# Performance work log

Hardware: AMD Instinct MI355X
Metric: run time of the kernel (lower is better)

The kernel has to match this reference:

```python
import jax, jax.numpy as jnp
import numpy as np

B, D, H, L = 2, 1024, 16, 4
BLK = 16                 # block_size == max_text_tokens
MT, MF = 16, 2032        # max_text_tokens, max_font_tokens
S = MT + MF              # 2048
NB = S // BLK            # 128 blocks
V = 490                  # font_vocab_size
HD = D // H              # 64
WIN = 30                 # 3*max_glyph_tokens/block_size = 3*160/16
NGLOB, NRAND = 1, 2      # BigBird global / random blocks
SOS = 0.42


def _make_layout():
    # Deterministic BigBird block layout per head: [H, NB, NB] bool
    rng = np.random.default_rng(0)
    layout = np.zeros((H, NB, NB), dtype=bool)
    layout[:, :NGLOB, :] = True          # global rows
    layout[:, :, :NGLOB] = True          # global cols
    for i in range(NB):                  # sliding window
        layout[:, i, max(0, i - WIN // 2):min(NB, i + WIN // 2 + 1)] = True
    for h in range(H):                   # random blocks
        for i in range(NB):
            layout[h, i, rng.choice(NB, size=NRAND, replace=False)] = True
    return jnp.asarray(layout)


def setup_inputs() -> dict:
    key = jax.random.key(0)
    ks = jax.random.split(key, 16)
    p = lambda k, shape: (0.02 * jax.random.normal(k, shape)).astype(jnp.float32)
    return {
        "text_embeddings": jax.random.normal(ks[0], (B, MT, D), jnp.float32),
        "font_embeddings": jax.random.normal(ks[1], (B, MF, D), jnp.float32),
        "layout": _make_layout(),
        "Wq": p(ks[2], (L, D, D)), "bq": jnp.zeros((L, D), jnp.float32),
        "Wk": p(ks[3], (L, D, D)), "bk": jnp.zeros((L, D), jnp.float32),
        "Wv": p(ks[4], (L, D, D)), "bv": jnp.zeros((L, D), jnp.float32),
        "Wo": p(ks[5], (L, D, D)), "bo": jnp.zeros((L, D), jnp.float32),
        "ln1_g": jnp.ones((L, D), jnp.float32), "ln1_b": jnp.zeros((L, D), jnp.float32),
        "ln2_g": jnp.ones((L, D), jnp.float32), "ln2_b": jnp.zeros((L, D), jnp.float32),
        "W1": p(ks[6], (L, D, 4 * D)), "b1": jnp.zeros((L, 4 * D), jnp.float32),
        "W2": p(ks[7], (L, 4 * D, D)), "b2": jnp.zeros((L, D), jnp.float32),
        "lnf_g": jnp.ones((D,), jnp.float32), "lnf_b": jnp.zeros((D,), jnp.float32),
        "Wout": p(ks[8], (D, V)),
    }


def _ln(x, g, b, eps=1e-5):
    mu = x.mean(-1, keepdims=True)
    var = ((x - mu) ** 2).mean(-1, keepdims=True)
    return (x - mu) * jax.lax.rsqrt(var + eps) * g + b


def _forward(text_embeddings, font_embeddings, layout, Wq, bq, Wk, bk, Wv, bv, Wo, bo,
             ln1_g, ln1_b, ln2_g, ln2_b, W1, b1, W2, b2, lnf_g, lnf_b, Wout):
    sos = jnp.full((B, 1, D), SOS, text_embeddings.dtype)
    x = jnp.concatenate([sos, text_embeddings, font_embeddings[:, :-1, :]], axis=1)  # [B,S,D]
    # token-level mask = block-sparse BigBird layout AND causal -> [H,S,S]
    tok_mask = jnp.repeat(jnp.repeat(layout, BLK, axis=1), BLK, axis=2)
    tok_mask = tok_mask & jnp.tril(jnp.ones((S, S), bool))[None]
    neg = jnp.asarray(-1e9, x.dtype)
    scale = jnp.asarray(1.0 / np.sqrt(HD), x.dtype)

    def layer(x, p):
        wq, bq_, wk, bk_, wv, bv_, wo, bo_, g1, gb1, g2, gb2, w1, bb1, w2, bb2 = p
        q = (x @ wq + bq_).reshape(B, S, H, HD).transpose(0, 2, 1, 3)
        k = (x @ wk + bk_).reshape(B, S, H, HD).transpose(0, 2, 1, 3)
        v = (x @ wv + bv_).reshape(B, S, H, HD).transpose(0, 2, 1, 3)
        scores = jnp.einsum('bhqd,bhkd->bhqk', q, k) * scale
        scores = jnp.where(tok_mask[None], scores, neg)
        probs = jax.nn.softmax(scores, axis=-1)
        a = jnp.einsum('bhqk,bhkd->bhqd', probs, v).transpose(0, 2, 1, 3).reshape(B, S, D)
        a = a @ wo + bo_
        x = _ln(x + a, g1, gb1)                                   # post-norm residual
        m = jax.nn.gelu(x @ w1 + bb1, approximate=False) @ w2 + bb2  # dropout=eval no-op
        x = _ln(x + m, g2, gb2)
        return x, None

    params = (Wq, bq, Wk, bk, Wv, bv, Wo, bo, ln1_g, ln1_b, ln2_g, ln2_b, W1, b1, W2, b2)
    x, _ = jax.lax.scan(jax.checkpoint(layer), x, params)
    logits = _ln(x, lnf_g, lnf_b) @ Wout                          # [B,S,V]
    return logits[:, :MT, :], logits[:, MT:, :]


def reference(text_embeddings, font_embeddings, layout, Wq, bq, Wk, bk, Wv, bv, Wo, bo,
              ln1_g, ln1_b, ln2_g, ln2_b, W1, b1, W2, b2, lnf_g, lnf_b, Wout):
    return _forward(text_embeddings, font_embeddings, layout, Wq, bq, Wk, bk, Wv, bv, Wo, bo,
                    ln1_g, ln1_b, ln2_g, ln2_b, W1, b1, W2, b2, lnf_g, lnf_b, Wout)
```

## Files before the change

kernel.cpp:

```cpp
#include <hip/hip_runtime.h>
#include <hip/hip_bf16.h>
#include <math.h>


typedef __hip_bfloat16 bf16;
typedef __attribute__((ext_vector_type(8))) short bf16x8;
typedef __attribute__((ext_vector_type(8))) unsigned short us8;
typedef __attribute__((ext_vector_type(4))) unsigned short us4;
typedef __attribute__((ext_vector_type(4))) float f32x4;
typedef __attribute__((ext_vector_type(8))) _Float16 f16x8;

#define S_LEN 2048
#define D_MODEL 1024
#define NBLK 128
#define NHEAD 16
#define BATCH 2
#define M_ROWS 4096
#define VOCAB 490

__device__ __forceinline__ float ldw(const void* p, size_t i, bool bf) {
    return bf ? __bfloat162float(((const bf16*)p)[i]) : ((const float*)p)[i];
}
__device__ __forceinline__ bool is_bf(const unsigned* probe) {
    return probe[0] != 0x3F800000u;
}
__device__ __forceinline__ unsigned short f2b(float f) {
    union { float f; unsigned u; } x; x.f = f;
    return (unsigned short)((x.u + 0x7FFFu + ((x.u >> 16) & 1u)) >> 16);
}
__device__ __forceinline__ unsigned short f2h(float f) {
    union { _Float16 h; unsigned short u; } x; x.h = (_Float16)f;
    return x.u;
}
__device__ __forceinline__ unsigned packh(float a, float b) {
    return (unsigned)f2h(a) | ((unsigned)f2h(b) << 16);
}
__device__ __forceinline__ float gelu_exact(float v) {
    float z = fabsf(v) * 0.70710678118654752f;
    float t = __builtin_amdgcn_rcpf(fmaf(0.3275911f, z, 1.f));
    float p = t * fmaf(t, fmaf(t, fmaf(t, fmaf(t, 1.061405429f, -1.453152027f),
                  1.421413741f), -0.284496736f), 0.254829592f);
    float er = 1.f - p * __expf(-z * z);
    er = copysignf(er, v);
    return 0.5f * v * (1.f + er);
}

__global__ __launch_bounds__(256) void norm_layout_kernel(
    const unsigned char* __restrict__ lraw, unsigned char* __restrict__ mask)
{
    int i = blockIdx.x * 256 + threadIdx.x;
    bool bytes_mode = (lraw[1] == 1);
    unsigned char v;
    if (bytes_mode) v = lraw[i] ? 1 : 0;
    else            v = ((const unsigned*)lraw)[i] ? 1 : 0;
    mask[i] = v;
}

__global__ __launch_bounds__(256) void build_x_kernel(
    const void* __restrict__ text, const void* __restrict__ font,
    float* __restrict__ x, unsigned short* __restrict__ xb,
    const unsigned* __restrict__ probe)
{
    bool bf = is_bf(probe);
    size_t idx = (size_t)blockIdx.x * 256 + threadIdx.x;
    int d = (int)(idx & 1023);
    int s = (int)((idx >> 10) & 2047);
    int b = (int)(idx >> 21);
    float v;
    if (s == 0)       v = bf ? 0.419921875f : 0.42f;
    else if (s <= 16) v = ldw(text, ((size_t)(b * 16 + (s - 1))) * 1024 + d, bf);
    else              v = ldw(font, ((size_t)(b * 2032 + (s - 17))) * 1024 + d, bf);
    x[idx] = v;
    xb[idx] = f2b(v);
}

__global__ __launch_bounds__(256) void transw_kernel(
    const void* __restrict__ W, size_t wOff, unsigned short* __restrict__ Wt,
    int K, int N, const unsigned* __restrict__ probe)
{
    bool bf = is_bf(probe);
    __shared__ unsigned short tile[32][36];
    int k0 = blockIdx.x * 32, n0 = blockIdx.y * 32;
    int t = threadIdx.x;
    int r  = t >> 3;
    int c4 = (t & 7) * 4;
    int n = n0 + c4;
    us4 tv;
    if (n + 4 <= N) {
        if (bf) {
            tv = *(const us4*)((const unsigned short*)W + wOff + (size_t)(k0 + r) * N + n);
        } else {
            float4 f = *(const float4*)((const float*)W + wOff + (size_t)(k0 + r) * N + n);
            tv = (us4){ f2b(f.x), f2b(f.y), f2b(f.z), f2b(f.w) };
        }
    } else {
        #pragma unroll
        for (int i = 0; i < 4; ++i)
            tv[i] = (n + i < N) ? f2b(ldw(W, wOff + (size_t)(k0 + r) * N + n + i, bf))
                                : (unsigned short)0;
    }
    *(us4*)(&tile[r][c4]) = tv;
    __syncthreads();
    int rn = t >> 3;
    int k4 = (t & 7) * 4;
    us4 ov = { tile[k4 + 0][rn], tile[k4 + 1][rn], tile[k4 + 2][rn], tile[k4 + 3][rn] };
    *(us4*)(&Wt[(size_t)(n0 + rn) * K + k0 + k4]) = ov;
}

__global__ __launch_bounds__(256) void transw4_kernel(
    const void* __restrict__ Wa, const void* __restrict__ Wb,
    const void* __restrict__ Wc, const void* __restrict__ Wd,
    size_t wOff, unsigned short* __restrict__ wt,
    const unsigned* __restrict__ probe)
{
    bool bf = is_bf(probe);
    int z = blockIdx.z;
    const void* W = z == 0 ? Wa : (z == 1 ? Wb : (z == 2 ? Wc : Wd));
    unsigned short* Wt = wt + (size_t)z * (1u << 20);
    __shared__ unsigned short tile[32][36];
    int k0 = blockIdx.x * 32, n0 = blockIdx.y * 32;
    int t = threadIdx.x;
    int r  = t >> 3;
    int c4 = (t & 7) * 4;
    us4 tv;
    if (bf) {
        tv = *(const us4*)((const unsigned short*)W + wOff + (size_t)(k0 + r) * 1024 + n0 + c4);
    } else {
        float4 f = *(const float4*)((const float*)W + wOff + (size_t)(k0 + r) * 1024 + n0 + c4);
        tv = (us4){ f2b(f.x), f2b(f.y), f2b(f.z), f2b(f.w) };
    }
    *(us4*)(&tile[r][c4]) = tv;
    __syncthreads();
    int rn = t >> 3;
    int k4 = (t & 7) * 4;
    us4 ov = { tile[k4 + 0][rn], tile[k4 + 1][rn], tile[k4 + 2][rn], tile[k4 + 3][rn] };
    *(us4*)(&Wt[(size_t)(n0 + rn) * 1024 + k0 + k4]) = ov;
}

__global__ __launch_bounds__(512) void gemm_kernel(
    const unsigned short* __restrict__ Ab,
    const unsigned short* __restrict__ Wt, size_t wtStride,
    const void* __restrict__ b0, const void* __restrict__ b1p, const void* __restrict__ b2p,
    size_t bOff,
    float* __restrict__ C0, float* __restrict__ C1, float* __restrict__ C2,
    void* __restrict__ Cb0, void* __restrict__ Cb1, void* __restrict__ Cb2,
    float* __restrict__ Cp,
    int M, int N, int K, int act, int outmode, const unsigned* __restrict__ probe)
{
    bool bf = is_bf(probe);
    __shared__ __align__(16) unsigned short As[2][128 * 64];
    __shared__ __align__(16) unsigned short Bs[2][128 * 64];

    int t    = threadIdx.x;
    int lane = t & 63;
    int wid  = t >> 6;
    int wm   = wid >> 2;
    int wn   = wid & 3;

    int gx  = gridDim.x;
    int gy  = gridDim.y;
    int bid = blockIdx.y * gx + blockIdx.x;
    int mi, ni;
    if (gy == 32 && (gx & 3) == 0) {
        int xcd = bid & 7, c = bid >> 3;
        int xr = xcd >> 2, xc = xcd & 3;
        int rw = gx >> 2;
        mi = xr * 16 + (c & 15);
        ni = xc * rw + (c >> 4);
    } else {
        int nwg = gx * gy;
        int swz = (bid & 7) * (nwg >> 3) + (bid >> 3);
        mi = swz / gx; ni = swz % gx;
    }
    int m0  = mi * 128;
    int n0t = ni * 128;
    int sel = n0t / N;
    int n0  = n0t - sel * N;
    int zz  = blockIdx.z;
    int Kit = K / gridDim.z;
    int kbase = zz * Kit;

    const void* bias = sel == 0 ? b0 : (sel == 1 ? b1p : b2p);
    float* C         = sel == 0 ? C0 : (sel == 1 ? C1 : C2);
    void* Cb         = sel == 0 ? Cb0 : (sel == 1 ? Cb1 : Cb2);
    const unsigned short* Wtb = Wt + (size_t)sel * wtStride;
    const bool vtr = (outmode == 3 && sel == 2);

    f32x4 acc[4][2];
    #pragma unroll
    for (int i = 0; i < 4; i++)
        #pragma unroll
        for (int j = 0; j < 2; j++)
            acc[i][j] = (f32x4){0.f, 0.f, 0.f, 0.f};

    const int fm = lane & 15;

    auto stageA = [&](int bb, int kt) {
        int k0 = kbase + (kt << 6);
        #pragma unroll
        for (int c = 0; c < 2; ++c) {
            int p    = (wid * 2 + c) * 64 + lane;
            int row  = p >> 3;
            int cp   = p & 7;
            int csrc = cp ^ (row & 7);
            const unsigned short* src = Ab + (size_t)(m0 + row) * K + k0 + csrc * 8;
            unsigned short* dst = &As[bb][(wid * 2 + c) * 512];
            __builtin_amdgcn_global_load_lds(
                (const __attribute__((address_space(1))) unsigned int*)src,
                (__attribute__((address_space(3))) unsigned int*)dst, 16, 0, 0);
        }
    };
    auto stageB = [&](int bb, int kt) {
        int k0 = kbase + (kt << 6);
        #pragma unroll
        for (int c = 0; c < 2; ++c) {
            int p    = (wid * 2 + c) * 64 + lane;
            int row  = p >> 3;
            int cp   = p & 7;
            int csrc = cp ^ (row & 7);
            const unsigned short* src = Wtb + (size_t)(n0 + row) * K + k0 + csrc * 8;
            unsigned short* dst = &Bs[bb][(wid * 2 + c) * 512];
            __builtin_amdgcn_global_load_lds(
                (const __attribute__((address_space(1))) unsigned int*)src,
                (__attribute__((address_space(3))) unsigned int*)dst, 16, 0, 0);
        }
    };
    auto compute = [&](int bb) {
        #pragma unroll
        for (int kk = 0; kk < 2; ++kk) {
            int cq = kk * 4 + (lane >> 4);
            bf16x8 af[4], bfr[2];
            #pragma unroll
            for (int i = 0; i < 4; ++i) {
                int r = wm * 64 + i * 16 + fm;
                af[i] = *(const bf16x8*)(&As[bb][r * 64 + (cq ^ (r & 7)) * 8]);
            }
            #pragma unroll
            for (int j = 0; j < 2; ++j) {
                int n = wn * 32 + j * 16 + fm;
                bfr[j] = *(const bf16x8*)(&Bs[bb][n * 64 + (cq ^ (n & 7)) * 8]);
            }
            #pragma unroll
            for (int i = 0; i < 4; ++i)
                #pragma unroll
                for (int j = 0; j < 2; ++j)
                    acc[i][j] = __builtin_amdgcn_mfma_f32_16x16x32_bf16(
                        af[i], bfr[j], acc[i][j], 0, 0, 0);
        }
    };

    int nt = Kit >> 6;
    stageA(0, 0);
    stageB(0, 0);
    __syncthreads();

    for (int kt = 0; kt < nt; ++kt) {
        int cur = kt & 1;
        bool more = (kt + 1) < nt;
        if (more) { stageA(cur ^ 1, kt + 1); stageB(cur ^ 1, kt + 1); }
        compute(cur);
        __syncthreads();
    }

    int rq = (lane >> 4) * 4;
    #pragma unroll
    for (int j = 0; j < 2; ++j) {
        int n = n0 + wn * 32 + j * 16 + fm;
        if (n >= N) continue;
        float bv = (bias && zz == 0) ? ldw(bias, bOff + n, bf) : 0.f;
        #pragma unroll
        for (int i = 0; i < 4; ++i) {
            int mb = m0 + wm * 64 + i * 16 + rq;
            if (zz > 0) {
                #pragma unroll
                for (int r = 0; r < 4; ++r)
                    Cp[(size_t)(mb + r) * N + n] = acc[i][j][r];
                continue;
            }
            if (vtr) {
                us4 o;
                #pragma unroll
                for (int r = 0; r < 4; ++r) o[r] = f2h(acc[i][j][r] + bv);
                int bb2 = mb >> 11, s0 = mb & 2047, hh = n >> 6, dd = n & 63;
                *(us4*)(&((unsigned short*)Cb)[((((size_t)(bb2 * 16 + hh)) * 64 + dd) << 11) + s0]) = o;
                continue;
            }
            #pragma unroll
            for (int r = 0; r < 4; ++r) {
                int m = mb + r;
                float v = acc[i][j][r] + bv;
                if (act == 1) v = gelu_exact(v);
                if (outmode == 0) {
                    C[(size_t)m * N + n] = v;
                } else if (outmode == 2) {
                    ((unsigned short*)Cb)[(size_t)m * N + n] = f2b(v);
                } else if (outmode == 3) {
                    ((unsigned short*)Cb)[(size_t)m * N + n] = f2h(v);
                } else {
                    int b = m >> 11;
                    int s = m & 2047;
                    size_t dst;
                    if (s < 16) dst = ((size_t)(b * 16 + s)) * N + n;
                    else        dst = (size_t)(BATCH * 16) * N + ((size_t)(b * 2032 + (s - 16))) * N + n;
                    if (bf) ((unsigned short*)Cb)[dst] = f2b(v);
                    else    ((float*)Cb)[dst] = v;
                }
            }
        }
    }
}

__global__ __launch_bounds__(256) void attn_kernel(
    const unsigned short* __restrict__ q16, const unsigned short* __restrict__ k16,
    const unsigned short* __restrict__ v16t, const unsigned char* __restrict__ mask,
    unsigned short* __restrict__ ab)
{
    int qgrp = (S_LEN / 64 - 1) - blockIdx.x;
    int h = blockIdx.y, b = blockIdx.z;

    __shared__ __align__(16) unsigned short ksd[64 * 64];
    __shared__ __align__(16) unsigned short vst[64 * 64];
    __shared__ unsigned char cflag[33];
    __shared__ unsigned char aclist[33];
    __shared__ int nac;

    int t = threadIdx.x, lane = t & 63, w = t >> 6;
    int qb = qgrp * 4 + w;
    const int fm = lane & 15, rq = lane >> 4;

    const unsigned char* mrow0 = mask + ((size_t)h * NBLK) * NBLK;

    if (t <= qgrp) {
        int jc = t;
        bool f = false;
        #pragma unroll
        for (int mb = 0; mb < 4; ++mb) {
            int j = jc * 4 + mb;
            #pragma unroll
            for (int ww = 0; ww < 4; ++ww) {
                int qq = qgrp * 4 + ww;
                f = f || ((j <= qq) && mrow0[qq * NBLK + j]);
            }
        }
        cflag[jc] = f ? 1 : 0;
    }
    __syncthreads();
    if (t == 0) {
        int n = 0;
        for (int jc = 0; jc <= qgrp; ++jc)
            if (cflag[jc]) aclist[n++] = (unsigned char)jc;
        nac = n;
    }

    int qrow = qb * 16 + fm;
    size_t qbase = ((size_t)(b * S_LEN + qrow)) * D_MODEL + h * 64;
    f16x8 qf0 = *(const f16x8*)(q16 + qbase + rq * 8);
    f16x8 qf1 = *(const f16x8*)(q16 + qbase + 32 + rq * 8);

    f32x4 O[4];
    #pragma unroll
    for (int c = 0; c < 4; ++c) O[c] = (f32x4){0.f, 0.f, 0.f, 0.f};
    float m_run = -1e30f, l_run = 0.f;
    const f16x8 hzero = (f16x8){0,0,0,0,0,0,0,0};

    __syncthreads();
    int nacl = nac;

    const int srow = t >> 2;
    const int sg   = (t & 3) * 2;
    const size_t vtbase = ((size_t)(b * NHEAD + h) * 64) * S_LEN;
    us8 kr0, kr1, vr0, vr1;

    auto loadKV = [&](int jc) {
        size_t kb = ((size_t)(b * S_LEN + jc * 64 + srow)) * D_MODEL + h * 64 + sg * 8;
        kr0 = *(const us8*)(k16 + kb);
        kr1 = *(const us8*)(k16 + kb + 8);
        size_t vb_ = vtbase + (size_t)srow * S_LEN + jc * 64 + sg * 8;
        vr0 = *(const us8*)(v16t + vb_);
        vr1 = *(const us8*)(v16t + vb_ + 8);
    };
    auto writeKV = [&]() {
        int p0 = (sg) ^ (srow & 7), p1 = (sg + 1) ^ (srow & 7);
        *(us8*)(&ksd[srow * 64 + p0 * 8]) = kr0;
        *(us8*)(&ksd[srow * 64 + p1 * 8]) = kr1;
        *(us8*)(&vst[srow * 64 + p0 * 8]) = vr0;
        *(us8*)(&vst[srow * 64 + p1 * 8]) = vr1;
    };

    if (nacl > 0) loadKV(aclist[0]);

    for (int ci = 0; ci < nacl; ++ci) {
        int jc = aclist[ci];
        __syncthreads();
        writeKV();
        if (ci + 1 < nacl) loadKV(aclist[ci + 1]);
        __syncthreads();

        #pragma unroll
        for (int mb = 0; mb < 4; ++mb) {
            int j = jc * 4 + mb;
            bool actv = (j <= qb) && mrow0[qb * NBLK + j];
            if (!actv) continue;

            int krow = mb * 16 + fm;
            f16x8 kf0 = *(const f16x8*)(&ksd[krow * 64 + ((0 * 4 + rq) ^ (krow & 7)) * 8]);
            f16x8 kf1 = *(const f16x8*)(&ksd[krow * 64 + ((1 * 4 + rq) ^ (krow & 7)) * 8]);
            f32x4 st = (f32x4){0.f, 0.f, 0.f, 0.f};
            st = __builtin_amdgcn_mfma_f32_16x16x32_f16(kf0, qf0, st, 0, 0, 0);
            st = __builtin_amdgcn_mfma_f32_16x16x32_f16(kf1, qf1, st, 0, 0, 0);

            float s[4];
            #pragma unroll
            for (int r = 0; r < 4; ++r) {
                s[r] = st[r] * 0.125f;
                if (j == qb && (rq * 4 + r) > fm) s[r] = -1e30f;
            }
            float mx = fmaxf(fmaxf(s[0], s[1]), fmaxf(s[2], s[3]));
            mx = fmaxf(mx, __shfl_xor(mx, 16));
            mx = fmaxf(mx, __shfl_xor(mx, 32));
            mx = fmaxf(m_run, mx);
            float al = __expf(m_run - mx);
            float p[4]; float ls = 0.f;
            #pragma unroll
            for (int r = 0; r < 4; ++r) {
                p[r] = (s[r] < -1e29f) ? 0.f : __expf(s[r] - mx);
                ls += p[r];
            }
            ls += __shfl_xor(ls, 16);
            ls += __shfl_xor(ls, 32);
            l_run = l_run * al + ls;
            m_run = mx;

            unsigned ph01 = packh(p[0], p[1]), ph23 = packh(p[2], p[3]);
            int s0 = fm + (((rq & 1) * 2) << 4);
            int s1 = s0 + 16;
            unsigned w0 = __shfl(ph01, s0), w1 = __shfl(ph23, s0);
            unsigned w2 = __shfl(ph01, s1), w3 = __shfl(ph23, s1);
            union { unsigned u[4]; f16x8 v; } pcv;
            pcv.u[0] = w0; pcv.u[1] = w1; pcv.u[2] = w2; pcv.u[3] = w3;
            f16x8 pa = (rq < 2) ? pcv.v : hzero;

            float al0 = __shfl(al, rq * 4 + 0), al1 = __shfl(al, rq * 4 + 1);
            float al2 = __shfl(al, rq * 4 + 2), al3 = __shfl(al, rq * 4 + 3);
            #pragma unroll
            for (int c = 0; c < 4; ++c) {
                O[c][0] *= al0; O[c][1] *= al1; O[c][2] *= al2; O[c][3] *= al3;
                f16x8 vb = hzero;
                if (rq < 2) {
                    int vrow = c * 16 + fm;
                    vb = *(const f16x8*)(&vst[vrow * 64 + ((mb * 2 + rq) ^ (vrow & 7)) * 8]);
                }
                O[c] = __builtin_amdgcn_mfma_f32_16x16x32_f16(pa, vb, O[c], 0, 0, 0);
            }
        }
    }

    float li0 = 1.f / __shfl(l_run, rq * 4 + 0);
    float li1 = 1.f / __shfl(l_run, rq * 4 + 1);
    float li2 = 1.f / __shfl(l_run, rq * 4 + 2);
    float li3 = 1.f / __shfl(l_run, rq * 4 + 3);
    size_t obase = ((size_t)(b * S_LEN + qb * 16)) * D_MODEL + h * 64;
    #pragma unroll
    for (int c = 0; c < 4; ++c) {
        ab[obase + (size_t)(rq * 4 + 0) * D_MODEL + c * 16 + fm] = f2b(O[c][0] * li0);
        ab[obase + (size_t)(rq * 4 + 1) * D_MODEL + c * 16 + fm] = f2b(O[c][1] * li1);
        ab[obase + (size_t)(rq * 4 + 2) * D_MODEL + c * 16 + fm] = f2b(O[c][2] * li2);
        ab[obase + (size_t)(rq * 4 + 3) * D_MODEL + c * 16 + fm] = f2b(O[c][3] * li3);
    }
}

__global__ __launch_bounds__(256) void add_ln_kernel(
    const float* __restrict__ xin, const float* __restrict__ res,
    const float* __restrict__ res2,
    float* __restrict__ xout, unsigned short* __restrict__ bfout,
    const void* __restrict__ g, size_t gOff,
    const void* __restrict__ bt, size_t bOff, const unsigned* __restrict__ probe)
{
    bool bf = is_bf(probe);
    int row = blockIdx.x;
    int t = threadIdx.x;
    __shared__ float red[4];

    float4 xv = ((const float4*)(xin + (size_t)row * D_MODEL))[t];
    if (res) {
        float4 rv = ((const float4*)(res + (size_t)row * D_MODEL))[t];
        xv.x += rv.x; xv.y += rv.y; xv.z += rv.z; xv.w += rv.w;
    }
    if (res2) {
        float4 rv = ((const float4*)(res2 + (size_t)row * D_MODEL))[t];
        xv.x += rv.x; xv.y += rv.y; xv.z += rv.z; xv.w += rv.w;
    }
    float s = xv.x + xv.y + xv.z + xv.w;
    for (int off = 32; off > 0; off >>= 1) s += __shfl_down(s, off);
    if ((t & 63) == 0) red[t >> 6] = s;
    __syncthreads();
    float mu = (red[0] + red[1] + red[2] + red[3]) * (1.f / 1024.f);
    __syncthreads();

    float d0 = xv.x - mu, d1 = xv.y - mu, d2 = xv.z - mu, d3 = xv.w - mu;
    float s2 = d0 * d0 + d1 * d1 + d2 * d2 + d3 * d3;
    for (int off = 32; off > 0; off >>= 1) s2 += __shfl_down(s2, off);
    if ((t & 63) == 0) red[t >> 6] = s2;
    __syncthreads();
    float var = (red[0] + red[1] + red[2] + red[3]) * (1.f / 1024.f);
    float rstd = rsqrtf(var + 1e-5f);

    int dbase = t * 4;
    float4 ov;
    ov.x = d0 * rstd * ldw(g, gOff + dbase + 0, bf) + ldw(bt, bOff + dbase + 0, bf);
    ov.y = d1 * rstd * ldw(g, gOff + dbase + 1, bf) + ldw(bt, bOff + dbase + 1, bf);
    ov.z = d2 * rstd * ldw(g, gOff + dbase + 2, bf) + ldw(bt, bOff + dbase + 2, bf);
    ov.w = d3 * rstd * ldw(g, gOff + dbase + 3, bf) + ldw(bt, bOff + dbase + 3, bf);
    ((float4*)(xout + (size_t)row * D_MODEL))[t] = ov;
    if (bfout) {
        us4 bv = { f2b(ov.x), f2b(ov.y), f2b(ov.z), f2b(ov.w) };
        *(us4*)(bfout + (size_t)row * D_MODEL + dbase) = bv;
    }
}

extern "C" void kernel_launch(void* const* d_in, const int* in_sizes, int n_in,
                              void* d_out, int out_size, void* d_ws, size_t ws_size,
                              hipStream_t stream) {
    const void* text  = d_in[0];
    const void* font  = d_in[1];
    const unsigned char* lraw = (const unsigned char*)d_in[2];
    const void* Wq    = d_in[3];
    const void* bq    = d_in[4];
    const void* Wk    = d_in[5];
    const void* bk    = d_in[6];
    const void* Wv    = d_in[7];
    const void* bv    = d_in[8];
    const void* Wo    = d_in[9];
    const void* bo_   = d_in[10];
    const void* ln1g  = d_in[11];
    const void* ln1b  = d_in[12];
    const void* ln2g  = d_in[13];
    const void* ln2b  = d_in[14];
    const void* W1    = d_in[15];
    const void* b1    = d_in[16];
    const void* W2    = d_in[17];
    const void* b2    = d_in[18];
    const void* lnfg  = d_in[19];
    const void* lnfb  = d_in[20];
    const void* Wout  = d_in[21];
    const unsigned* probe = (const unsigned*)d_in[11];

    const size_t Q = (size_t)M_ROWS * D_MODEL;
    float* ws = (float*)d_ws;
    float* x  = ws;
    float* G0 = ws + Q;
    unsigned short* q16 = (unsigned short*)(ws + 2 * Q);
    unsigned short* k16 = q16 + Q;
    unsigned short* v16 = k16 + Q;
    unsigned short* hb  = (unsigned short*)(ws + 2 * Q);
    unsigned short* xb  = (unsigned short*)(ws + 4 * Q);
    unsigned short* ab  = (unsigned short*)(ws + 4 * Q + Q / 2);
    unsigned char* mask = (unsigned char*)(ws + 5 * Q);
    unsigned short* wt  = (unsigned short*)((char*)d_ws + 5 * Q * 4 + 262144);

    const size_t baseEnd = 5 * Q * 4 + 262144 + 8 * ((size_t)1 << 20) * 2;
    bool canSplit = ws_size >= baseEnd + Q * 4;
    float* part = (float*)((char*)d_ws + baseEnd);

    norm_layout_kernel<<<(NHEAD * NBLK * NBLK) / 256, 256, 0, stream>>>(lraw, mask);
    build_x_kernel<<<(BATCH * S_LEN * D_MODEL) / 256, 256, 0, stream>>>(text, font, x, xb, probe);

    dim3 gQKV(3 * D_MODEL / 128, M_ROWS / 128);
    dim3 gD(D_MODEL / 128, M_ROWS / 128, canSplit ? 2 : 1);
    dim3 gF(4 * D_MODEL / 128, M_ROWS / 128);
    dim3 gV((VOCAB + 127) / 128, M_ROWS / 128);

    const size_t MSZ = (size_t)1 << 20;
    const float* r2 = canSplit ? part : nullptr;

    for (int l = 0; l < 4; l++) {
        size_t wo  = (size_t)l * D_MODEL * D_MODEL;
        size_t bo1 = (size_t)l * D_MODEL;
        size_t w1o = (size_t)l * D_MODEL * 4 * D_MODEL;
        size_t b1o = (size_t)l * 4 * D_MODEL;

        transw4_kernel<<<dim3(32, 32, 4), 256, 0, stream>>>(Wq, Wk, Wv, Wo, wo, wt, probe);

        gemm_kernel<<<gQKV, 512, 0, stream>>>(xb, wt, MSZ, bq, bk, bv, bo1,
                                              nullptr, nullptr, nullptr, q16, k16, v16,
                                              nullptr,
                                              M_ROWS, D_MODEL, D_MODEL, 0, 3, probe);
        attn_kernel<<<dim3(S_LEN / 64, NHEAD, BATCH), 256, 0, stream>>>(
            q16, k16, v16, mask, ab);
        gemm_kernel<<<gD, 512, 0, stream>>>(ab, wt + 3 * MSZ, 0, bo_, bo_, bo_, bo1,
                                            G0, G0, G0, nullptr, nullptr, nullptr,
                                            part,
                                            M_ROWS, D_MODEL, D_MODEL, 0, 0, probe);
        add_ln_kernel<<<M_ROWS, 256, 0, stream>>>(x, G0, r2, x, xb, ln1g, bo1, ln1b, bo1, probe);

        transw_kernel<<<dim3(32, 128), 256, 0, stream>>>(W1, w1o, wt, D_MODEL, 4 * D_MODEL, probe);
        transw_kernel<<<dim3(128, 32), 256, 0, stream>>>(W2, w1o, wt + 4 * MSZ, 4 * D_MODEL, D_MODEL, probe);

        gemm_kernel<<<gF, 512, 0, stream>>>(xb, wt, 0, b1, b1, b1, b1o,
                                            nullptr, nullptr, nullptr, hb, hb, hb,
                                            nullptr,
                                            M_ROWS, 4 * D_MODEL, D_MODEL, 1, 2, probe);
        gemm_kernel<<<gD, 512, 0, stream>>>(hb, wt + 4 * MSZ, 0, b2, b2, b2, bo1,
                                            G0, G0, G0, nullptr, nullptr, nullptr,
                                            part,
                                            M_ROWS, D_MODEL, 4 * D_MODEL, 0, 0, probe);
        add_ln_kernel<<<M_ROWS, 256, 0, stream>>>(x, G0, r2, x, xb, ln2g, bo1, ln2b, bo1, probe);
    }

    add_ln_kernel<<<M_ROWS, 256, 0, stream>>>(x, nullptr, nullptr, G0, ab, lnfg, 0, lnfb, 0, probe);
    transw_kernel<<<dim3(32, 16), 256, 0, stream>>>(Wout, 0, wt, D_MODEL, VOCAB, probe);
    gemm_kernel<<<gV, 512, 0, stream>>>(ab, wt, 0, nullptr, nullptr, nullptr, 0,
                                        nullptr, nullptr, nullptr, d_out, d_out, d_out,
                                        nullptr,
                                        M_ROWS, VOCAB, D_MODEL, 0, 1, probe);
}
```

Before: 1.286 ms.

## Batch all weight transposes into one upfront kernel and skip unneeded softmax rescales

```diff
diff --git a/kernel.cpp b/kernel.cpp
--- a/kernel.cpp
+++ b/kernel.cpp
@@ -74,14 +74,11 @@
     xb[idx] = f2b(v);
 }
 
-__global__ __launch_bounds__(256) void transw_kernel(
-    const void* __restrict__ W, size_t wOff, unsigned short* __restrict__ Wt,
-    int K, int N, const unsigned* __restrict__ probe)
-{
-    bool bf = is_bf(probe);
+__device__ __forceinline__ void transw_tile(
+    const void* W, size_t wOff, unsigned short* Wt,
+    int K, int N, int k0, int n0, int t, bool bf)
+{
     __shared__ unsigned short tile[32][36];
-    int k0 = blockIdx.x * 32, n0 = blockIdx.y * 32;
-    int t = threadIdx.x;
     int r  = t >> 3;
     int c4 = (t & 7) * 4;
     int n = n0 + c4;
@@ -107,34 +104,58 @@
     *(us4*)(&Wt[(size_t)(n0 + rn) * K + k0 + k4]) = ov;
 }
 
+__global__ __launch_bounds__(256) void transw_kernel(
+    const void* __restrict__ W, size_t wOff, unsigned short* __restrict__ Wt,
+    int K, int N, const unsigned* __restrict__ probe)
+{
+    transw_tile(W, wOff, Wt, K, N, blockIdx.x * 32, blockIdx.y * 32,
+                threadIdx.x, is_bf(probe));
+}
+
 __global__ __launch_bounds__(256) void transw4_kernel(
     const void* __restrict__ Wa, const void* __restrict__ Wb,
     const void* __restrict__ Wc, const void* __restrict__ Wd,
     size_t wOff, unsigned short* __restrict__ wt,
     const unsigned* __restrict__ probe)
 {
-    bool bf = is_bf(probe);
     int z = blockIdx.z;
     const void* W = z == 0 ? Wa : (z == 1 ? Wb : (z == 2 ? Wc : Wd));
-    unsigned short* Wt = wt + (size_t)z * (1u << 20);
-    __shared__ unsigned short tile[32][36];
-    int k0 = blockIdx.x * 32, n0 = blockIdx.y * 32;
-    int t = threadIdx.x;
-    int r  = t >> 3;
-    int c4 = (t & 7) * 4;
-    us4 tv;
-    if (bf) {
-        tv = *(const us4*)((const unsigned short*)W + wOff + (size_t)(k0 + r) * 1024 + n0 + c4);
+    transw_tile(W, wOff, wt + (size_t)z * (1u << 20), 1024, 1024,
+                blockIdx.x * 32, blockIdx.y * 32, threadIdx.x, is_bf(probe));
+}
+
+__global__ __launch_bounds__(256) void transw_all_kernel(
+    const void* __restrict__ Wq, const void* __restrict__ Wk,
+    const void* __restrict__ Wv, const void* __restrict__ Wo,
+    const void* __restrict__ W1, const void* __restrict__ W2,
+    const void* __restrict__ Wout, unsigned short* __restrict__ wtAll,
+    const unsigned* __restrict__ probe)
+{
+    bool bf = is_bf(probe);
+    int pid = blockIdx.x;
+    const size_t M1 = (size_t)1 << 20;
+    if (pid < 49152) {
+        int l = pid / 12288, r = pid % 12288;
+        unsigned short* base = wtAll + (size_t)l * 12 * M1;
+        if (r < 4096) {
+            int z = r >> 10, q = r & 1023;
+            const void* W = z == 0 ? Wq : (z == 1 ? Wk : (z == 2 ? Wv : Wo));
+            transw_tile(W, (size_t)l * 1024 * 1024, base + (size_t)z * M1,
+                        1024, 1024, (q & 31) * 32, (q >> 5) * 32, threadIdx.x, bf);
+        } else if (r < 8192) {
+            int q = r - 4096;
+            transw_tile(W1, (size_t)l * 1024 * 4096, base + 4 * M1,
+                        1024, 4096, (q & 31) * 32, (q >> 5) * 32, threadIdx.x, bf);
+        } else {
+            int q = r - 8192;
+            transw_tile(W2, (size_t)l * 1024 * 4096, base + 8 * M1,
+                        4096, 1024, (q & 127) * 32, (q >> 7) * 32, threadIdx.x, bf);
+        }
     } else {
-        float4 f = *(const float4*)((const float*)W + wOff + (size_t)(k0 + r) * 1024 + n0 + c4);
-        tv = (us4){ f2b(f.x), f2b(f.y), f2b(f.z), f2b(f.w) };
-    }
-    *(us4*)(&tile[r][c4]) = tv;
-    __syncthreads();
-    int rn = t >> 3;
-    int k4 = (t & 7) * 4;
-    us4 ov = { tile[k4 + 0][rn], tile[k4 + 1][rn], tile[k4 + 2][rn], tile[k4 + 3][rn] };
-    *(us4*)(&Wt[(size_t)(n0 + rn) * 1024 + k0 + k4]) = ov;
+        int q = pid - 49152;
+        transw_tile(Wout, 0, wtAll + 48 * M1,
+                    1024, VOCAB, (q & 31) * 32, (q >> 5) * 32, threadIdx.x, bf);
+    }
 }
 
 __global__ __launch_bounds__(512) void gemm_kernel(
@@ -415,11 +436,11 @@
                 s[r] = st[r] * 0.125f;
                 if (j == qb && (rq * 4 + r) > fm) s[r] = -1e30f;
             }
-            float mx = fmaxf(fmaxf(s[0], s[1]), fmaxf(s[2], s[3]));
-            mx = fmaxf(mx, __shfl_xor(mx, 16));
-            mx = fmaxf(mx, __shfl_xor(mx, 32));
-            mx = fmaxf(m_run, mx);
-            float al = __expf(m_run - mx);
+            float bm = fmaxf(fmaxf(s[0], s[1]), fmaxf(s[2], s[3]));
+            bm = fmaxf(bm, __shfl_xor(bm, 16));
+            bm = fmaxf(bm, __shfl_xor(bm, 32));
+            bool noresc = __all(bm <= m_run + 8.f);
+            float mx = noresc ? m_run : fmaxf(m_run, bm);
             float p[4]; float ls = 0.f;
             #pragma unroll
             for (int r = 0; r < 4; ++r) {
@@ -428,8 +449,6 @@
             }
             ls += __shfl_xor(ls, 16);
             ls += __shfl_xor(ls, 32);
-            l_run = l_run * al + ls;
-            m_run = mx;
 
             unsigned ph01 = packh(p[0], p[1]), ph23 = packh(p[2], p[3]);
             int s0 = fm + (((rq & 1) * 2) << 4);
@@ -440,11 +459,21 @@
             pcv.u[0] = w0; pcv.u[1] = w1; pcv.u[2] = w2; pcv.u[3] = w3;
             f16x8 pa = (rq < 2) ? pcv.v : hzero;
 
-            float al0 = __shfl(al, rq * 4 + 0), al1 = __shfl(al, rq * 4 + 1);
-            float al2 = __shfl(al, rq * 4 + 2), al3 = __shfl(al, rq * 4 + 3);
+            if (noresc) {
+                l_run += ls;
+            } else {
+                float al = __expf(m_run - mx);
+                l_run = l_run * al + ls;
+                m_run = mx;
+                float al0 = __shfl(al, rq * 4 + 0), al1 = __shfl(al, rq * 4 + 1);
+                float al2 = __shfl(al, rq * 4 + 2), al3 = __shfl(al, rq * 4 + 3);
+                #pragma unroll
+                for (int c = 0; c < 4; ++c) {
+                    O[c][0] *= al0; O[c][1] *= al1; O[c][2] *= al2; O[c][3] *= al3;
+                }
+            }
             #pragma unroll
             for (int c = 0; c < 4; ++c) {
-                O[c][0] *= al0; O[c][1] *= al1; O[c][2] *= al2; O[c][3] *= al3;
                 f16x8 vb = hzero;
                 if (rq < 2) {
                     int vrow = c * 16 + fm;
@@ -561,16 +590,23 @@
     const size_t baseEnd = 5 * Q * 4 + 262144 + 8 * ((size_t)1 << 20) * 2;
     bool canSplit = ws_size >= baseEnd + Q * 4;
     float* part = (float*)((char*)d_ws + baseEnd);
+    const size_t M1 = (size_t)1 << 20;
+    const size_t allEnd = baseEnd + Q * 4;
+    bool canAll = ws_size >= allEnd + 2 * (48 * M1 + (M1 >> 1));
+    unsigned short* wtAll = (unsigned short*)((char*)d_ws + allEnd);
 
     norm_layout_kernel<<<(NHEAD * NBLK * NBLK) / 256, 256, 0, stream>>>(lraw, mask);
     build_x_kernel<<<(BATCH * S_LEN * D_MODEL) / 256, 256, 0, stream>>>(text, font, x, xb, probe);
+    if (canAll)
+        transw_all_kernel<<<49664, 256, 0, stream>>>(Wq, Wk, Wv, Wo, W1, W2, Wout,
+                                                     wtAll, probe);
 
     dim3 gQKV(3 * D_MODEL / 128, M_ROWS / 128);
     dim3 gD(D_MODEL / 128, M_ROWS / 128, canSplit ? 2 : 1);
     dim3 gF(4 * D_MODEL / 128, M_ROWS / 128);
     dim3 gV((VOCAB + 127) / 128, M_ROWS / 128);
 
-    const size_t MSZ = (size_t)1 << 20;
+    const size_t MSZ = M1;
     const float* r2 = canSplit ? part : nullptr;
 
     for (int l = 0; l < 4; l++) {
@@ -579,28 +615,36 @@
         size_t w1o = (size_t)l * D_MODEL * 4 * D_MODEL;
         size_t b1o = (size_t)l * 4 * D_MODEL;
 
-        transw4_kernel<<<dim3(32, 32, 4), 256, 0, stream>>>(Wq, Wk, Wv, Wo, wo, wt, probe);
-
-        gemm_kernel<<<gQKV, 512, 0, stream>>>(xb, wt, MSZ, bq, bk, bv, bo1,
+        unsigned short* qkvW = canAll ? (wtAll + (size_t)l * 12 * M1) : wt;
+        unsigned short* woW  = canAll ? (wtAll + (size_t)l * 12 * M1 + 3 * M1) : (wt + 3 * MSZ);
+        unsigned short* w1W  = canAll ? (wtAll + (size_t)l * 12 * M1 + 4 * M1) : wt;
+        unsigned short* w2W  = canAll ? (wtAll + (size_t)l * 12 * M1 + 8 * M1) : (wt + 4 * MSZ);
+
+        if (!canAll)
+            transw4_kernel<<<dim3(32, 32, 4), 256, 0, stream>>>(Wq, Wk, Wv, Wo, wo, wt, probe);
+
+        gemm_kernel<<<gQKV, 512, 0, stream>>>(xb, qkvW, MSZ, bq, bk, bv, bo1,
                                               nullptr, nullptr, nullptr, q16, k16, v16,
                                               nullptr,
                                               M_ROWS, D_MODEL, D_MODEL, 0, 3, probe);
         attn_kernel<<<dim3(S_LEN / 64, NHEAD, BATCH), 256, 0, stream>>>(
             q16, k16, v16, mask, ab);
-        gemm_kernel<<<gD, 512, 0, stream>>>(ab, wt + 3 * MSZ, 0, bo_, bo_, bo_, bo1,
+        gemm_kernel<<<gD, 512, 0, stream>>>(ab, woW, 0, bo_, bo_, bo_, bo1,
                                             G0, G0, G0, nullptr, nullptr, nullptr,
                                             part,
                                             M_ROWS, D_MODEL, D_MODEL, 0, 0, probe);
         add_ln_kernel<<<M_ROWS, 256, 0, stream>>>(x, G0, r2, x, xb, ln1g, bo1, ln1b, bo1, probe);
 
-        transw_kernel<<<dim3(32, 128), 256, 0, stream>>>(W1, w1o, wt, D_MODEL, 4 * D_MODEL, probe);
-        transw_kernel<<<dim3(128, 32), 256, 0, stream>>>(W2, w1o, wt + 4 * MSZ, 4 * D_MODEL, D_MODEL, probe);
-
-        gemm_kernel<<<gF, 512, 0, stream>>>(xb, wt, 0, b1, b1, b1, b1o,
+        if (!canAll) {
+            transw_kernel<<<dim3(32, 128), 256, 0, stream>>>(W1, w1o, wt, D_MODEL, 4 * D_MODEL, probe);
+            transw_kernel<<<dim3(128, 32), 256, 0, stream>>>(W2, w1o, wt + 4 * MSZ, 4 * D_MODEL, D_MODEL, probe);
+        }
+
+        gemm_kernel<<<gF, 512, 0, stream>>>(xb, w1W, 0, b1, b1, b1, b1o,
                                             nullptr, nullptr, nullptr, hb, hb, hb,
                                             nullptr,
                                             M_ROWS, 4 * D_MODEL, D_MODEL, 1, 2, probe);
-        gemm_kernel<<<gD, 512, 0, stream>>>(hb, wt + 4 * MSZ, 0, b2, b2, b2, bo1,
+        gemm_kernel<<<gD, 512, 0, stream>>>(hb, w2W, 0, b2, b2, b2, bo1,
                                             G0, G0, G0, nullptr, nullptr, nullptr,
                                             part,
                                             M_ROWS, D_MODEL, 4 * D_MODEL, 0, 0, probe);
@@ -608,8 +652,10 @@
     }
 
     add_ln_kernel<<<M_ROWS, 256, 0, stream>>>(x, nullptr, nullptr, G0, ab, lnfg, 0, lnfb, 0, probe);
-    transw_kernel<<<dim3(32, 16), 256, 0, stream>>>(Wout, 0, wt, D_MODEL, VOCAB, probe);
-    gemm_kernel<<<gV, 512, 0, stream>>>(ab, wt, 0, nullptr, nullptr, nullptr, 0,
+    unsigned short* headW = canAll ? (wtAll + 48 * M1) : wt;
+    if (!canAll)
+        transw_kernel<<<dim3(32, 16), 256, 0, stream>>>(Wout, 0, wt, D_MODEL, VOCAB, probe);
+    gemm_kernel<<<gV, 512, 0, stream>>>(ab, headW, 0, nullptr, nullptr, nullptr, 0,
                                         nullptr, nullptr, nullptr, d_out, d_out, d_out,
                                         nullptr,
                                         M_ROWS, VOCAB, D_MODEL, 0, 1, probe);
```

After: 1.311 ms. About the same (+1.9%).
